# Optimization experiments

Measured on AMD Instinct MI355X. Metric: run time of the kernel, lower is better.

## Reference

```python
import jax, jax.numpy as jnp
import numpy as np

N = 100000
E = 600000
IN_DIM = 128
HID = 128


def setup_inputs() -> dict:
    key = jax.random.key(0)
    ks = jax.random.split(key, 12)
    def lin(kw, fan_in, fan_out):
        # torch nn.Linear default init: U(-1/sqrt(fan_in), 1/sqrt(fan_in))
        bound = 1.0 / np.sqrt(fan_in)
        kw1, kw2 = jax.random.split(kw)
        w = jax.random.uniform(kw1, (fan_in, fan_out), jnp.float32, -bound, bound)
        b = jax.random.uniform(kw2, (fan_out,), jnp.float32, -bound, bound)
        return w, b
    x = jax.random.normal(ks[0], (N, IN_DIM), jnp.float32)
    edge_index = jax.random.randint(ks[1], (2, E), 0, N, jnp.int64)
    w1a, b1a = lin(ks[2], IN_DIM, HID)
    w1b, b1b = lin(ks[3], HID, HID)
    w2a, b2a = lin(ks[4], HID, HID)
    w2b, b2b = lin(ks[5], HID, HID)
    wo, bo = lin(ks[6], HID, 1)
    return {"x": x, "edge_index": edge_index,
            "w1a": w1a, "b1a": b1a, "w1b": w1b, "b1b": b1b,
            "w2a": w2a, "b2a": b2a, "w2b": w2b, "b2b": b2b,
            "wo": wo, "bo": bo}


def _gin_conv(x, src, dst, wa, ba, wb, bb):
    # sum-aggregate neighbor features: agg[dst] += x[src]; eps = 0 (GIN default)
    agg = jax.ops.segment_sum(x[src], dst, num_segments=N)
    h = x + agg
    h = jax.nn.relu(h @ wa + ba)
    return h @ wb + bb


def reference(x, edge_index, w1a, b1a, w1b, b1b, w2a, b2a, w2b, b2b, wo, bo):
    src, dst = edge_index[0], edge_index[1]
    h = _gin_conv(x, src, dst, w1a, b1a, w1b, b1b)
    h = _gin_conv(h, src, dst, w2a, b2a, w2b, b2b)
    return (h @ wo + bo).squeeze(-1)  # [N]
```

## Files before the change

### kernel.cpp

```cpp
#include <hip/hip_runtime.h>

typedef unsigned short u16;
typedef unsigned int u32;
typedef __bf16 bf16x8 __attribute__((ext_vector_type(8)));
typedef float f32x4 __attribute__((ext_vector_type(4)));

#define CAP 32

__device__ __forceinline__ u16 f2bf(float f) {
  union { float f; u32 u; } c; c.f = f;
  return (u16)((c.u + 0x7fffu + ((c.u >> 16) & 1u)) >> 16);
}
__device__ __forceinline__ float2 upk2(u32 v) {
  union { u32 u; float f; } a, b; a.u = v << 16; b.u = v & 0xffff0000u;
  return make_float2(a.f, b.f);
}
__device__ __forceinline__ u32 pk2(float x, float y) {
  return (u32)f2bf(x) | ((u32)f2bf(y) << 16);
}

__global__ __launch_bounds__(256) void k_prep2(const float4* __restrict__ x4,
                                               uint2* __restrict__ xb,
                                               int n4, int castBlocks, int trBlocks,
                                               const float* __restrict__ w0,
                                               const float* __restrict__ w1,
                                               const float* __restrict__ w2,
                                               const float* __restrict__ w3,
                                               u16* __restrict__ wT,
                                               int* __restrict__ cursor, int N) {
  int b = blockIdx.x, t = threadIdx.x;
  if (b < castBlocks) {
    int i = b * 256 + t;
    if (i < n4) {
      float4 v = x4[i];
      xb[i] = make_uint2(pk2(v.x, v.y), pk2(v.z, v.w));
    }
  } else if (b < castBlocks + trBlocks) {
    int id = (b - castBlocks) * 256 + t;
    int w = id >> 14, rem = id & 16383;
    int nn = rem >> 7, kk = rem & 127;
    const float* s = (w == 0) ? w0 : (w == 1) ? w1 : (w == 2) ? w2 : w3;
    wT[id] = f2bf(s[kk * 128 + nn]);
  } else {
    int i = (b - castBlocks - trBlocks) * 256 + t;
    if (i < N) cursor[i] = 0;
  }
}

__global__ __launch_bounds__(256) void k_fillp(const int* __restrict__ src,
                                               const int* __restrict__ dst,
                                               int* __restrict__ cursor,
                                               int* __restrict__ edge_src, int E) {
  int e = blockIdx.x * 256 + threadIdx.x;
  if (e < E) {
    int d = dst[e];
    int pos = atomicAdd(&cursor[d], 1);
    if (pos < CAP) edge_src[d * CAP + pos] = src[e];
  }
}

__global__ __launch_bounds__(256) void k_agg(const uint4* __restrict__ in,
                                             uint4* __restrict__ out,
                                             const int* __restrict__ cursor,
                                             const int* __restrict__ edge_src, int N) {
  int lane = threadIdx.x & 63;
  int g = lane >> 4, l = lane & 15;
  int wid = blockIdx.x * 4 + (threadIdx.x >> 6);
  int node = wid * 4 + g;
  bool valid = node < N;
  int nc = valid ? node : (N - 1);

  int2 e = *(const int2*)&edge_src[nc * CAP + 2 * l];
  int cnt = cursor[nc];
  uint4 sv = in[(size_t)nc * 16 + l];

  cnt = valid ? cnt : 0;
  cnt = (cnt < CAP) ? cnt : CAP;

  float acc[8];
#pragma unroll
  for (int i = 0; i < 8; ++i) acc[i] = 0.f;

  auto fma8 = [&](uint4 v, float w) {
    float2 p;
    p = upk2(v.x); acc[0] = fmaf(w, p.x, acc[0]); acc[1] = fmaf(w, p.y, acc[1]);
    p = upk2(v.y); acc[2] = fmaf(w, p.x, acc[2]); acc[3] = fmaf(w, p.y, acc[3]);
    p = upk2(v.z); acc[4] = fmaf(w, p.x, acc[4]); acc[5] = fmaf(w, p.y, acc[5]);
    p = upk2(v.w); acc[6] = fmaf(w, p.x, acc[6]); acc[7] = fmaf(w, p.y, acc[7]);
  };

  fma8(sv, 1.f);

  for (int b = 0; b < cnt; b += 8) {
    uint4 v[8];
#pragma unroll
    for (int k = 0; k < 8; ++k) {
      int idx = __shfl((k & 1) ? e.y : e.x, (g << 4) + (b >> 1) + (k >> 1), 64);
      bool act = (b + k) < cnt;
      int p = act ? idx : nc;
      v[k] = in[(size_t)p * 16 + l];
    }
#pragma unroll
    for (int k = 0; k < 8; ++k) fma8(v[k], ((b + k) < cnt) ? 1.f : 0.f);
  }

  if (valid) {
    uint4 o;
    o.x = pk2(acc[0], acc[1]);
    o.y = pk2(acc[2], acc[3]);
    o.z = pk2(acc[4], acc[5]);
    o.w = pk2(acc[6], acc[7]);
    out[(size_t)node * 16 + l] = o;
  }
}

template <bool HEAD>
__global__ __launch_bounds__(256) void k_mlp(const u16* __restrict__ in,
                                             const u16* __restrict__ wAT,
                                             const float* __restrict__ bA,
                                             const u16* __restrict__ wBT,
                                             const float* __restrict__ bB,
                                             const float* __restrict__ wo,
                                             const float* __restrict__ bo,
                                             void* __restrict__ outp,
                                             int N, int ntiles) {
  __shared__ u16 lA[64 * 128];
  __shared__ u16 lW[2 * 128 * 128];
  const int tid = threadIdx.x;
  const int wave = tid >> 6, lane = tid & 63;
  const int m16 = lane & 15, quad = lane >> 4;

#pragma unroll
  for (int it = 0; it < 16; ++it) {
    int id = it * 256 + tid;
    int m = id >> 11, rem = id & 2047;
    int row = rem >> 4, c = rem & 15;
    const u16* s = m ? wBT : wAT;
    uint4 v = *(const uint4*)&s[row * 128 + c * 8];
    *(uint4*)&lW[m * 16384 + row * 128 + ((c ^ (row & 15)) << 3)] = v;
  }

  float bAr[8], bBr[8], woR[8], bBh[8];
#pragma unroll
  for (int t = 0; t < 8; ++t) {
    bAr[t] = bA[t * 16 + m16];
    bBr[t] = HEAD ? 0.f : bB[t * 16 + m16];
    woR[t] = HEAD ? wo[t * 16 + m16] : 0.f;
    bBh[t] = HEAD ? bB[t * 16 + m16] : 0.f;
  }
  float boV = HEAD ? bo[0] : 0.f;

  __syncthreads();

  const int mrow = wave * 16 + m16;

  uint4 pf[4];
  auto gload = [&](int tl) {
#pragma unroll
    for (int it = 0; it < 4; ++it) {
      int gr = tl * 64 + wave * 16 + it * 4 + quad;
      uint4 v = make_uint4(0u, 0u, 0u, 0u);
      if (gr < N) v = *(const uint4*)&in[(size_t)gr * 128 + m16 * 8];
      pf[it] = v;
    }
  };

  int tile = blockIdx.x;
  if (tile < ntiles) gload(tile);
  for (; tile < ntiles; tile += gridDim.x) {
#pragma unroll
    for (int it = 0; it < 4; ++it) {
      int row = wave * 16 + it * 4 + quad;
      *(uint4*)&lA[row * 128 + ((m16 ^ (row & 15)) << 3)] = pf[it];
    }
    bf16x8 aF[4];
#pragma unroll
    for (int ks = 0; ks < 4; ++ks)
      aF[ks] = *(const bf16x8*)&lA[mrow * 128 + (((ks * 4 + quad) ^ m16) << 3)];
    int nxt = tile + gridDim.x;
    if (nxt < ntiles) gload(nxt);

    f32x4 acc[8];
#pragma unroll
    for (int t = 0; t < 8; ++t) acc[t] = (f32x4){0.f, 0.f, 0.f, 0.f};
#pragma unroll
    for (int t = 0; t < 8; ++t) {
      int nrow = t * 16 + m16;
#pragma unroll
      for (int ks = 0; ks < 4; ++ks) {
        bf16x8 bF = *(const bf16x8*)&lW[nrow * 128 + (((ks * 4 + quad) ^ m16) << 3)];
        acc[t] = __builtin_amdgcn_mfma_f32_16x16x32_bf16(aF[ks], bF, acc[t], 0, 0, 0);
      }
    }
#pragma unroll
    for (int t = 0; t < 8; ++t) {
      int n = t * 16 + m16;
#pragma unroll
      for (int r = 0; r < 4; ++r) {
        int rloc = quad * 4 + r;
        int absrow = wave * 16 + rloc;
        float v = acc[t][r] + bAr[t];
        v = v > 0.f ? v : 0.f;
        lA[absrow * 128 + ((((n >> 3) ^ rloc) << 3) | (n & 7))] = f2bf(v);
      }
    }
#pragma unroll
    for (int ks = 0; ks < 4; ++ks)
      aF[ks] = *(const bf16x8*)&lA[mrow * 128 + (((ks * 4 + quad) ^ m16) << 3)];
#pragma unroll
    for (int t = 0; t < 8; ++t) acc[t] = (f32x4){0.f, 0.f, 0.f, 0.f};
#pragma unroll
    for (int t = 0; t < 8; ++t) {
      int nrow = t * 16 + m16;
#pragma unroll
      for (int ks = 0; ks < 4; ++ks) {
        bf16x8 bF = *(const bf16x8*)&lW[16384 + nrow * 128 + (((ks * 4 + quad) ^ m16) << 3)];
        acc[t] = __builtin_amdgcn_mfma_f32_16x16x32_bf16(aF[ks], bF, acc[t], 0, 0, 0);
      }
    }
    if (!HEAD) {
#pragma unroll
      for (int t = 0; t < 8; ++t) {
        int n = t * 16 + m16;
#pragma unroll
        for (int r = 0; r < 4; ++r) {
          int rloc = quad * 4 + r;
          int absrow = wave * 16 + rloc;
          float v = acc[t][r] + bBr[t];
          lA[absrow * 128 + ((((n >> 3) ^ rloc) << 3) | (n & 7))] = f2bf(v);
        }
      }
      u16* out = (u16*)outp;
#pragma unroll
      for (int it = 0; it < 4; ++it) {
        int row = wave * 16 + it * 4 + quad;
        int gr = tile * 64 + row;
        if (gr < N) {
          uint4 v = *(const uint4*)&lA[row * 128 + ((m16 ^ (row & 15)) << 3)];
          *(uint4*)&out[(size_t)gr * 128 + m16 * 8] = v;
        }
      }
    } else {
      float* out = (float*)outp;
      float s[4];
#pragma unroll
      for (int r = 0; r < 4; ++r) {
        float v = 0.f;
#pragma unroll
        for (int t = 0; t < 8; ++t) v += (acc[t][r] + bBh[t]) * woR[t];
        s[r] = v;
      }
#pragma unroll
      for (int r = 0; r < 4; ++r) {
        s[r] += __shfl_xor(s[r], 1, 64);
        s[r] += __shfl_xor(s[r], 2, 64);
        s[r] += __shfl_xor(s[r], 4, 64);
        s[r] += __shfl_xor(s[r], 8, 64);
      }
      if (m16 == 0) {
#pragma unroll
        for (int r = 0; r < 4; ++r) {
          int gr = tile * 64 + wave * 16 + quad * 4 + r;
          if (gr < N) out[gr] = s[r] + boV;
        }
      }
    }
  }
}

extern "C" void kernel_launch(void* const* d_in, const int* in_sizes, int n_in,
                              void* d_out, int out_size, void* d_ws, size_t ws_size,
                              hipStream_t stream) {
  const float* x = (const float*)d_in[0];
  const int* ei = (const int*)d_in[1];
  const int E = in_sizes[1] / 2;
  const int N = in_sizes[0] / 128;
  const int* srcI = ei;
  const int* dstI = ei + E;
  const float* w1a = (const float*)d_in[2];
  const float* b1a = (const float*)d_in[3];
  const float* w1b = (const float*)d_in[4];
  const float* b1b = (const float*)d_in[5];
  const float* w2a = (const float*)d_in[6];
  const float* b2a = (const float*)d_in[7];
  const float* w2b = (const float*)d_in[8];
  const float* b2b = (const float*)d_in[9];
  const float* wo = (const float*)d_in[10];
  const float* bo = (const float*)d_in[11];

  char* ws = (char*)d_ws;
  size_t off = 0;
  auto nx = [&](size_t bytes) {
    size_t o = off;
    off += (bytes + 511) & ~(size_t)511;
    return o;
  };
  int* cursor   = (int*)(ws + nx((size_t)N * 4));
  int* edge_src = (int*)(ws + nx((size_t)N * CAP * 4));
  u16* wT       = (u16*)(ws + nx((size_t)4 * 16384 * 2));
  u16* xb       = (u16*)(ws + nx((size_t)N * 128 * 2));
  u16* bufA     = (u16*)(ws + nx((size_t)N * 128 * 2));
  u16* bufB     = (u16*)(ws + nx((size_t)N * 128 * 2));

  const int n4 = N * 32;
  const int castBlocks = (n4 + 255) / 256;
  const int trBlocks = 256;
  const int zeroBlocks = (N + 255) / 256;

  k_prep2<<<castBlocks + trBlocks + zeroBlocks, 256, 0, stream>>>(
      (const float4*)x, (uint2*)xb, n4, castBlocks, trBlocks,
      w1a, w1b, w2a, w2b, wT, cursor, N);
  k_fillp<<<(E + 255) / 256, 256, 0, stream>>>(srcI, dstI, cursor, edge_src, E);

  const int aggBlocks = (N + 15) / 16;
  const int ntiles = (N + 63) / 64;
  const int mlpGrid = 512;

  k_agg<<<aggBlocks, 256, 0, stream>>>((const uint4*)xb, (uint4*)bufA, cursor, edge_src, N);
  k_mlp<false><<<mlpGrid, 256, 0, stream>>>(bufA, wT, b1a, wT + 16384, b1b,
                                            nullptr, nullptr, bufB, N, ntiles);
  k_agg<<<aggBlocks, 256, 0, stream>>>((const uint4*)bufB, (uint4*)xb, cursor, edge_src, N);
  k_mlp<true><<<mlpGrid, 256, 0, stream>>>(xb, wT + 32768, b2a, wT + 49152, b2b,
                                           wo, bo, d_out, N, ntiles);
}
```

Before: 234.1 us.

## Fuse neighbor aggregation into MLP kernel and overlap gathers with MFMA

Removes the separate aggregation kernels and performs the neighbor sum inside the MLP kernel for each 64-row tile. The gather loads for the next tile are issued before the current tile's matrix math and consumed after it, so gather latency can overlap with compute. This drops the intermediate buffer write and read and two launches. The cost is more register pressure and lower occupancy in the fused kernel, and the gather is now spread over a persistent 512-block grid.

```diff
diff --git a/kernel.cpp b/kernel.cpp
--- a/kernel.cpp
+++ b/kernel.cpp
@@ -17,6 +17,13 @@
 }
 __device__ __forceinline__ u32 pk2(float x, float y) {
   return (u32)f2bf(x) | ((u32)f2bf(y) << 16);
+}
+__device__ __forceinline__ void fma8u(float* acc, uint4 v, float w) {
+  float2 p;
+  p = upk2(v.x); acc[0] = fmaf(w, p.x, acc[0]); acc[1] = fmaf(w, p.y, acc[1]);
+  p = upk2(v.y); acc[2] = fmaf(w, p.x, acc[2]); acc[3] = fmaf(w, p.y, acc[3]);
+  p = upk2(v.z); acc[4] = fmaf(w, p.x, acc[4]); acc[5] = fmaf(w, p.y, acc[5]);
+  p = upk2(v.w); acc[6] = fmaf(w, p.x, acc[6]); acc[7] = fmaf(w, p.y, acc[7]);
 }
 
 __global__ __launch_bounds__(256) void k_prep2(const float4* __restrict__ x4,
@@ -59,63 +66,10 @@
   }
 }
 
-__global__ __launch_bounds__(256) void k_agg(const uint4* __restrict__ in,
-                                             uint4* __restrict__ out,
-                                             const int* __restrict__ cursor,
-                                             const int* __restrict__ edge_src, int N) {
-  int lane = threadIdx.x & 63;
-  int g = lane >> 4, l = lane & 15;
-  int wid = blockIdx.x * 4 + (threadIdx.x >> 6);
-  int node = wid * 4 + g;
-  bool valid = node < N;
-  int nc = valid ? node : (N - 1);
-
-  int2 e = *(const int2*)&edge_src[nc * CAP + 2 * l];
-  int cnt = cursor[nc];
-  uint4 sv = in[(size_t)nc * 16 + l];
-
-  cnt = valid ? cnt : 0;
-  cnt = (cnt < CAP) ? cnt : CAP;
-
-  float acc[8];
-#pragma unroll
-  for (int i = 0; i < 8; ++i) acc[i] = 0.f;
-
-  auto fma8 = [&](uint4 v, float w) {
-    float2 p;
-    p = upk2(v.x); acc[0] = fmaf(w, p.x, acc[0]); acc[1] = fmaf(w, p.y, acc[1]);
-    p = upk2(v.y); acc[2] = fmaf(w, p.x, acc[2]); acc[3] = fmaf(w, p.y, acc[3]);
-    p = upk2(v.z); acc[4] = fmaf(w, p.x, acc[4]); acc[5] = fmaf(w, p.y, acc[5]);
-    p = upk2(v.w); acc[6] = fmaf(w, p.x, acc[6]); acc[7] = fmaf(w, p.y, acc[7]);
-  };
-
-  fma8(sv, 1.f);
-
-  for (int b = 0; b < cnt; b += 8) {
-    uint4 v[8];
-#pragma unroll
-    for (int k = 0; k < 8; ++k) {
-      int idx = __shfl((k & 1) ? e.y : e.x, (g << 4) + (b >> 1) + (k >> 1), 64);
-      bool act = (b + k) < cnt;
-      int p = act ? idx : nc;
-      v[k] = in[(size_t)p * 16 + l];
-    }
-#pragma unroll
-    for (int k = 0; k < 8; ++k) fma8(v[k], ((b + k) < cnt) ? 1.f : 0.f);
-  }
-
-  if (valid) {
-    uint4 o;
-    o.x = pk2(acc[0], acc[1]);
-    o.y = pk2(acc[2], acc[3]);
-    o.z = pk2(acc[4], acc[5]);
-    o.w = pk2(acc[6], acc[7]);
-    out[(size_t)node * 16 + l] = o;
-  }
-}
-
 template <bool HEAD>
 __global__ __launch_bounds__(256) void k_mlp(const u16* __restrict__ in,
+                                             const int* __restrict__ cursor,
+                                             const int* __restrict__ edge_src,
                                              const u16* __restrict__ wAT,
                                              const float* __restrict__ bA,
                                              const u16* __restrict__ wBT,
@@ -129,6 +83,7 @@
   const int tid = threadIdx.x;
   const int wave = tid >> 6, lane = tid & 63;
   const int m16 = lane & 15, quad = lane >> 4;
+  const uint4* in4 = (const uint4*)in;
 
 #pragma unroll
   for (int it = 0; it < 16; ++it) {
@@ -155,18 +110,71 @@
   const int mrow = wave * 16 + m16;
 
   uint4 pf[4];
-  auto gload = [&](int tl) {
+  int2 eL[4]; int cntL[4]; uint4 svL[4];
+
+  auto aissue = [&](int tl) {
 #pragma unroll
     for (int it = 0; it < 4; ++it) {
-      int gr = tl * 64 + wave * 16 + it * 4 + quad;
-      uint4 v = make_uint4(0u, 0u, 0u, 0u);
-      if (gr < N) v = *(const uint4*)&in[(size_t)gr * 128 + m16 * 8];
-      pf[it] = v;
-    }
+      int node = tl * 64 + wave * 16 + it * 4 + quad;
+      int nc = node < N ? node : N - 1;
+      eL[it] = *(const int2*)&edge_src[nc * CAP + 2 * m16];
+      cntL[it] = cursor[nc];
+      svL[it] = in4[(size_t)nc * 16 + m16];
+    }
+  };
+
+  auto gi = [&](int it, int cnt, uint4* v) {
+#pragma unroll
+    for (int k = 0; k < 8; ++k) {
+      int idx = __shfl((k & 1) ? eL[it].y : eL[it].x, (quad << 4) + (k >> 1), 64);
+      uint4 vv = make_uint4(0u, 0u, 0u, 0u);
+      if (k < cnt) vv = in4[(size_t)idx * 16 + m16];
+      v[k] = vv;
+    }
+  };
+  auto gc = [&](int it, int cnt, uint4* v, bool valid) {
+    float a8[8];
+#pragma unroll
+    for (int i = 0; i < 8; ++i) a8[i] = 0.f;
+    fma8u(a8, svL[it], valid ? 1.f : 0.f);
+#pragma unroll
+    for (int k = 0; k < 8; ++k) fma8u(a8, v[k], 1.f);
+    for (int b = 8; b < cnt; b += 8) {
+      uint4 w[8];
+#pragma unroll
+      for (int k = 0; k < 8; ++k) {
+        int idx = __shfl((k & 1) ? eL[it].y : eL[it].x, (quad << 4) + (b >> 1) + (k >> 1), 64);
+        uint4 vv = make_uint4(0u, 0u, 0u, 0u);
+        if (b + k < cnt) vv = in4[(size_t)idx * 16 + m16];
+        w[k] = vv;
+      }
+#pragma unroll
+      for (int k = 0; k < 8; ++k) fma8u(a8, w[k], 1.f);
+    }
+    pf[it] = make_uint4(pk2(a8[0], a8[1]), pk2(a8[2], a8[3]),
+                        pk2(a8[4], a8[5]), pk2(a8[6], a8[7]));
+  };
+
+  auto aconsume = [&](int tl) {
+    int base = tl * 64 + wave * 16 + quad;
+    bool v0 = base + 0 < N, v1 = base + 4 < N, v2 = base + 8 < N, v3 = base + 12 < N;
+    int c0 = v0 ? (cntL[0] < CAP ? cntL[0] : CAP) : 0;
+    int c1 = v1 ? (cntL[1] < CAP ? cntL[1] : CAP) : 0;
+    int c2 = v2 ? (cntL[2] < CAP ? cntL[2] : CAP) : 0;
+    int c3 = v3 ? (cntL[3] < CAP ? cntL[3] : CAP) : 0;
+    uint4 vA[8], vB[8];
+    gi(0, c0, vA);
+    gi(1, c1, vB);
+    gc(0, c0, vA, v0);
+    gi(2, c2, vA);
+    gc(1, c1, vB, v1);
+    gi(3, c3, vB);
+    gc(2, c2, vA, v2);
+    gc(3, c3, vB, v3);
   };
 
   int tile = blockIdx.x;
-  if (tile < ntiles) gload(tile);
+  if (tile < ntiles) { aissue(tile); aconsume(tile); }
   for (; tile < ntiles; tile += gridDim.x) {
 #pragma unroll
     for (int it = 0; it < 4; ++it) {
@@ -178,7 +186,7 @@
     for (int ks = 0; ks < 4; ++ks)
       aF[ks] = *(const bf16x8*)&lA[mrow * 128 + (((ks * 4 + quad) ^ m16) << 3)];
     int nxt = tile + gridDim.x;
-    if (nxt < ntiles) gload(nxt);
+    if (nxt < ntiles) aissue(nxt);
 
     f32x4 acc[8];
 #pragma unroll
@@ -265,6 +273,7 @@
         }
       }
     }
+    if (nxt < ntiles) aconsume(nxt);
   }
 }
 
@@ -299,7 +308,6 @@
   int* edge_src = (int*)(ws + nx((size_t)N * CAP * 4));
   u16* wT       = (u16*)(ws + nx((size_t)4 * 16384 * 2));
   u16* xb       = (u16*)(ws + nx((size_t)N * 128 * 2));
-  u16* bufA     = (u16*)(ws + nx((size_t)N * 128 * 2));
   u16* bufB     = (u16*)(ws + nx((size_t)N * 128 * 2));
 
   const int n4 = N * 32;
@@ -312,14 +320,13 @@
       w1a, w1b, w2a, w2b, wT, cursor, N);
   k_fillp<<<(E + 255) / 256, 256, 0, stream>>>(srcI, dstI, cursor, edge_src, E);
 
-  const int aggBlocks = (N + 15) / 16;
   const int ntiles = (N + 63) / 64;
   const int mlpGrid = 512;
 
-  k_agg<<<aggBlocks, 256, 0, stream>>>((const uint4*)xb, (uint4*)bufA, cursor, edge_src, N);
-  k_mlp<false><<<mlpGrid, 256, 0, stream>>>(bufA, wT, b1a, wT + 16384, b1b,
+  k_mlp<false><<<mlpGrid, 256, 0, stream>>>(xb, cursor, edge_src,
+                                            wT, b1a, wT + 16384, b1b,
                                             nullptr, nullptr, bufB, N, ntiles);
-  k_agg<<<aggBlocks, 256, 0, stream>>>((const uint4*)bufB, (uint4*)xb, cursor, edge_src, N);
-  k_mlp<true><<<mlpGrid, 256, 0, stream>>>(xb, wT + 32768, b2a, wT + 49152, b2b,
+  k_mlp<true><<<mlpGrid, 256, 0, stream>>>(bufB, cursor, edge_src,
+                                           wT + 32768, b2a, wT + 49152, b2b,
                                            wo, bo, d_out, N, ntiles);
 }
```

Result: no change. 231.7 us (-1.0%).
